# Kernel optimization log

Hardware: AMD Instinct MI355X
Metric: run time of the kernel (lower is better)

## Reference

```python
import jax, jax.numpy as jnp
import numpy as np

EPS = 1e-5  # BatchNorm1d default eps


def _gcn(h_in, W, b, src, dst, dinv):
    h = h_in @ W  # [N, D]
    coef = dinv[src] * dinv[dst]  # [E]
    agg = jax.ops.segment_sum(h[src] * coef[:, None], dst, num_segments=h.shape[0])
    agg = agg + h * (dinv * dinv)[:, None]  # self-loop contribution
    return agg + b


def _bn(h, gamma, beta):
    # training-mode BatchNorm1d over the node dimension (biased variance)
    mu = jnp.mean(h, axis=0)
    var = jnp.var(h, axis=0)
    return gamma * (h - mu) * jax.lax.rsqrt(var + EPS) + beta


def setup_inputs() -> dict:
    key = jax.random.key(0)
    N, E, F_IN, D, B = 50000, 800000, 64, 256, 1000
    ks = jax.random.split(key, 8)
    x = jax.random.normal(ks[0], (N, F_IN), dtype=jnp.float32)
    edge_index = jax.random.randint(ks[1], (2, E), 0, N)
    batch_index = (jnp.arange(N) * B) // N  # sorted, every graph non-empty (~50 nodes each)
    s = lambda k, sh: (jax.random.normal(k, sh, dtype=jnp.float32) * 0.05)
    inp = {
        "x": x, "edge_index": edge_index, "batch_index": batch_index, "num_graphs": B,
        "W0": s(ks[2], (F_IN, D)), "b0": jnp.zeros((D,), jnp.float32),
        "W1": s(ks[3], (D, D)), "b1": jnp.zeros((D,), jnp.float32),
        "W2": s(ks[4], (D, D)), "b2": jnp.zeros((D,), jnp.float32),
        "W3": s(ks[5], (D, D)), "b3": jnp.zeros((D,), jnp.float32),
        "g0": jnp.ones((D,), jnp.float32), "be0": jnp.zeros((D,), jnp.float32),
        "g1": jnp.ones((D,), jnp.float32), "be1": jnp.zeros((D,), jnp.float32),
        "g2": jnp.ones((D,), jnp.float32), "be2": jnp.zeros((D,), jnp.float32),
        "g3": jnp.ones((D,), jnp.float32), "be3": jnp.zeros((D,), jnp.float32),
        "Wout": s(ks[6], (2 * D, 1)), "bout": jnp.zeros((1,), jnp.float32),
    }
    return inp


def reference(x, edge_index, batch_index, num_graphs,
              W0, b0, W1, b1, W2, b2, W3, b3,
              g0, be0, g1, be1, g2, be2, g3, be3,
              Wout, bout):
    N = x.shape[0]
    src, dst = edge_index[0], edge_index[1]
    # degree after adding self-loops (all edge weights = 1)
    deg = 1.0 + jax.ops.segment_sum(jnp.ones(src.shape[0], x.dtype), dst, num_segments=N)
    dinv = jax.lax.rsqrt(deg)

    h = x
    for W, b, g, be in ((W0, b0, g0, be0), (W1, b1, g1, be1),
                        (W2, b2, g2, be2), (W3, b3, g3, be3)):
        h = jnp.tanh(_bn(_gcn(h, W, b, src, dst, dinv), g, be))

    # global max pool + global average pool over graphs
    hmax = jax.ops.segment_max(h, batch_index, num_segments=num_graphs)
    hsum = jax.ops.segment_sum(h, batch_index, num_segments=num_graphs)
    cnt = jax.ops.segment_sum(jnp.ones(N, x.dtype), batch_index, num_segments=num_graphs)
    hmean = hsum / cnt[:, None]
    hidden = jnp.concatenate([hmax, hmean], axis=1)  # [B, 512]
    out = hidden @ Wout + bout  # [B, 1]
    return (out, hidden)
```

## Files before the change

kernel.cpp:

```cpp
#include <hip/hip_runtime.h>
#include <hip/hip_bf16.h>
#include <math.h>

#define D 256
#define EPS 1e-5f
#define SCAN_NB 256

typedef _Float16 f16;
typedef _Float16 f16x4 __attribute__((ext_vector_type(4)));
typedef _Float16 f16x8 __attribute__((ext_vector_type(8)));
typedef float f32x4v __attribute__((ext_vector_type(4)));
typedef unsigned int uint;

__device__ __forceinline__ float fast_tanh(float x) {
    float e = __expf(2.f * x);
    return 1.f - __fdividef(2.f, e + 1.f);
}

union HU { f16 h; unsigned short u; };
__device__ __forceinline__ uint pack_rec(int s, float c) {
    HU hu; hu.h = (f16)c;
    return ((uint)s << 16) | (uint)hu.u;
}
__device__ __forceinline__ float rec_coef(uint r) {
    HU hu; hu.u = (unsigned short)(r & 0xffffu);
    return (float)hu.h;
}

__global__ void k_count(const int* __restrict__ dst, int* __restrict__ cnt,
                        int* __restrict__ rank, int E) {
    int e = blockIdx.x * blockDim.x + threadIdx.x;
    if (e < E) rank[e] = atomicAdd(&cnt[dst[e]], 1);
}

__global__ void k_scan_part(const int* __restrict__ cnt, int* __restrict__ row_ptr,
                            int* __restrict__ partial, int N, int C) {
    __shared__ int sdata[256];
    int b = blockIdx.x, t = threadIdx.x;
    int base = b * C;
    int end = base + C; if (end > N) end = N;
    int running = 0;
    for (int ts = base; ts < end; ts += 256) {
        int idx = ts + t;
        int val = (idx < end) ? cnt[idx] : 0;
        sdata[t] = val;
        __syncthreads();
        for (int s = 1; s < 256; s <<= 1) {
            int v = (t >= s) ? sdata[t - s] : 0;
            __syncthreads();
            sdata[t] += v;
            __syncthreads();
        }
        if (idx < end) row_ptr[idx] = running + sdata[t] - val;
        running += sdata[255];
        __syncthreads();
    }
    if (t == 0) partial[b] = running;
}

__global__ void k_scan_off(int* __restrict__ partial) {
    __shared__ int sdata[256];
    int t = threadIdx.x;
    int val = partial[t];
    sdata[t] = val;
    __syncthreads();
    for (int s = 1; s < 256; s <<= 1) {
        int v = (t >= s) ? sdata[t - s] : 0;
        __syncthreads();
        sdata[t] += v;
        __syncthreads();
    }
    partial[t] = sdata[t] - val;
}

__global__ void k_scan_add(int* __restrict__ row_ptr,
                           const int* __restrict__ partial, const int* __restrict__ cnt,
                           float* __restrict__ dinv, int N, int C, int E) {
    int i = blockIdx.x * 256 + threadIdx.x;
    if (i < N) {
        row_ptr[i] += partial[i / C];
        dinv[i] = rsqrtf(1.0f + (float)cnt[i]);
    }
    if (i == N) row_ptr[N] = E;
}

__global__ void k_fill(const int* __restrict__ src, const int* __restrict__ dst,
                       const int* __restrict__ rank, const int* __restrict__ row_ptr,
                       const float* __restrict__ dinv, uint* __restrict__ ecp, int E) {
    int e = blockIdx.x * blockDim.x + threadIdx.x;
    if (e >= E) return;
    int s = src[e], t = dst[e];
    ecp[row_ptr[t] + rank[e]] = pack_rec(s, dinv[s] * dinv[t]);
}

__global__ void k_cast(const float* __restrict__ in, f16* __restrict__ o, int n4,
                       float* __restrict__ sums, float* __restrict__ sumsq) {
    int i = blockIdx.x * 256 + threadIdx.x;
    if (blockIdx.x == 0) {
        sums[threadIdx.x]  = 0.f;
        sumsq[threadIdx.x] = 0.f;
    }
    if (i >= n4) return;
    float4 v = ((const float4*)in)[i];
    f16x4 h = {(f16)v.x, (f16)v.y, (f16)v.z, (f16)v.w};
    ((f16x4*)o)[i] = h;
}

__global__ void k_prep_w_all(const float* __restrict__ W0, const float* __restrict__ W1,
                             const float* __restrict__ W2, const float* __restrict__ W3,
                             f16* __restrict__ T0, f16* __restrict__ T1,
                             f16* __restrict__ T2, f16* __restrict__ T3) {
    int idx = blockIdx.x * 256 + threadIdx.x;
    if (idx < 16384) {
        int k = idx >> 8, d = idx & 255;
        T0[(size_t)d * 64 + k] = (f16)W0[idx];
        return;
    }
    idx -= 16384;
    const float* W; f16* T;
    if (idx < 65536)      { W = W1; T = T1; }
    else if (idx < 131072){ W = W2; T = T2; idx -= 65536; }
    else                  { W = W3; T = T3; idx -= 131072; }
    int k = idx >> 8, d = idx & 255;
    T[(size_t)d * 256 + k] = (f16)W[idx];
}

#define KSTEP 64
#define ATS 72
__global__ __launch_bounds__(256)
void k_gemm(const f16* __restrict__ A, const f16* __restrict__ Wt,
            f16* __restrict__ outh, int N, int K,
            float* __restrict__ sums, float* __restrict__ sumsq) {
    __shared__ __align__(16) f16 As[128 * ATS];
    __shared__ __align__(16) f16 Bs[128 * ATS];
    const int r0 = blockIdx.x * 128;
    const int c0 = blockIdx.y * 128;
    const int t = threadIdx.x;
    const int lane = t & 63, wave = t >> 6;
    const int wr = wave >> 1, wc = wave & 1;
    const int quad = lane >> 4, m = lane & 15;

    f32x4v acc[4][4];
#pragma unroll
    for (int i = 0; i < 4; ++i)
#pragma unroll
        for (int j = 0; j < 4; ++j) acc[i][j] = {0.f, 0.f, 0.f, 0.f};

    const int sr = t >> 1;
    const int sc0 = (t & 1) * 32;

    for (int k0 = 0; k0 < K; k0 += KSTEP) {
        int gr = r0 + sr;
        uint4 a[4];
#pragma unroll
        for (int u = 0; u < 4; ++u) a[u] = make_uint4(0u, 0u, 0u, 0u);
        if (gr < N) {
            const f16* ap = A + (size_t)gr * K + k0 + sc0;
#pragma unroll
            for (int u = 0; u < 4; ++u) a[u] = *(const uint4*)(ap + u * 8);
        }
#pragma unroll
        for (int u = 0; u < 4; ++u)
            *(uint4*)(As + sr * ATS + sc0 + u * 8) = a[u];
        const f16* bp = Wt + (size_t)(c0 + sr) * K + k0 + sc0;
#pragma unroll
        for (int u = 0; u < 4; ++u)
            *(uint4*)(Bs + sr * ATS + sc0 + u * 8) = *(const uint4*)(bp + u * 8);
        __syncthreads();

#pragma unroll
        for (int kk = 0; kk < KSTEP; kk += 32) {
            f16x8 af[4], bf[4];
#pragma unroll
            for (int i = 0; i < 4; ++i)
                af[i] = *(const f16x8*)(As + (wr * 64 + i * 16 + m) * ATS + kk + quad * 8);
#pragma unroll
            for (int j = 0; j < 4; ++j)
                bf[j] = *(const f16x8*)(Bs + (wc * 64 + j * 16 + m) * ATS + kk + quad * 8);
#pragma unroll
            for (int i = 0; i < 4; ++i)
#pragma unroll
                for (int j = 0; j < 4; ++j)
                    acc[i][j] = __builtin_amdgcn_mfma_f32_16x16x32_f16(af[i], bf[j], acc[i][j], 0, 0, 0);
        }
        __syncthreads();
    }

#pragma unroll
    for (int i = 0; i < 4; ++i) {
#pragma unroll
        for (int r = 0; r < 4; ++r) {
            int row = r0 + wr * 64 + i * 16 + quad * 4 + r;
            if (row < N) {
#pragma unroll
                for (int j = 0; j < 4; ++j) {
                    int colm = c0 + wc * 64 + j * 16 + m;
                    outh[(size_t)row * D + colm] = (f16)acc[i][j][r];
                }
            }
        }
    }

    {
        __shared__ float cs[128], css[128];
        if (t < 128) { cs[t] = 0.f; css[t] = 0.f; }
        __syncthreads();
#pragma unroll
        for (int j = 0; j < 4; ++j) {
            int f = wc * 64 + j * 16 + m;
            float s = 0.f, q = 0.f;
#pragma unroll
            for (int i = 0; i < 4; ++i)
#pragma unroll
                for (int r = 0; r < 4; ++r) {
                    float v = acc[i][j][r];
                    s += v; q += v * v;
                }
            atomicAdd(&cs[f], s);
            atomicAdd(&css[f], q);
        }
        __syncthreads();
        if (t < 128) {
            atomicAdd(&sums[c0 + t], cs[t]);
            atomicAdd(&sumsq[c0 + t], css[t]);
        }
    }
}

__global__ __launch_bounds__(256)
void k_gather_q(const int* __restrict__ row_ptr, const uint4* __restrict__ ecp4,
                const unsigned char* __restrict__ hq, const float* __restrict__ dinv,
                f16* __restrict__ out, float* __restrict__ sums,
                float* __restrict__ sumsq, float* __restrict__ scf_out,
                const float* __restrict__ scf_in, int N) {
    sums[threadIdx.x]  = 0.f;
    sumsq[threadIdx.x] = 0.f;

    const int lane = threadIdx.x & 63;
    const int wave = threadIdx.x >> 6;
    const uint* __restrict__ hqu = (const uint*)hq;
    f16x4* __restrict__ out4 = (f16x4*)out;

    const int wtotal = gridDim.x * 4;
    int i = blockIdx.x * 4 + wave;
    if (i >= N) return;

    int lo = row_ptr[i], hi = row_ptr[i + 1];
    float dv = dinv[i];
    float sci = scf_in ? scf_in[i] : 0.f;
    uint selfu = hqu[(uint)i * 64u + (uint)lane];

    while (true) {
        int inext = i + wtotal;
        int lo2 = 0, hi2 = 0; float dv2 = 0.f, sci2 = 0.f; uint su2 = 0u;
        if (inext < N) {
            lo2 = row_ptr[inext]; hi2 = row_ptr[inext + 1];
            dv2 = dinv[inext];
            if (scf_in) sci2 = scf_in[inext];
            su2 = hqu[(uint)inext * 64u + (uint)lane];
        }

        float dd = dv * dv;
        float scf = scf_in ? sci : dd;
        float4 acc;
        acc.x = (float)(selfu & 0xffu) * dd;
        acc.y = (float)((selfu >> 8) & 0xffu) * dd;
        acc.z = (float)((selfu >> 16) & 0xffu) * dd;
        acc.w = (float)(selfu >> 24) * dd;

        for (int e = (lo & ~3); e < hi; e += 8) {
            uint4 p0 = ecp4[(e >> 2)];
            uint4 p1 = ecp4[(e >> 2) + 1];
            uint pr[8] = {p0.x, p0.y, p0.z, p0.w, p1.x, p1.y, p1.z, p1.w};
            uint rv[8]; float cf[8];
            if ((e >= lo) & (e + 8 <= hi)) {
#pragma unroll
                for (int j = 0; j < 8; ++j) {
                    uint rec = __builtin_amdgcn_readfirstlane(pr[j]);
                    const uint* rp = hqu + ((rec >> 16) << 6);
                    rv[j] = rp[lane];
                    cf[j] = rec_coef(rec);
                }
            } else {
#pragma unroll
                for (int j = 0; j < 8; ++j) {
                    int ej = e + j;
                    bool v = (ej >= lo) & (ej < hi);
                    uint rec = __builtin_amdgcn_readfirstlane(pr[j]);
                    const uint* rp = hqu + ((rec >> 16) << 6);
                    rv[j] = rp[lane];
                    cf[j] = v ? rec_coef(rec) : 0.f;
                }
            }
#pragma unroll
            for (int j = 0; j < 8; ++j) {
                float c = cf[j];
                uint v = rv[j];
                acc.x = fmaf((float)(v & 0xffu), c, acc.x);
                acc.y = fmaf((float)((v >> 8) & 0xffu), c, acc.y);
                acc.z = fmaf((float)((v >> 16) & 0xffu), c, acc.z);
                acc.w = fmaf((float)(v >> 24), c, acc.w);
            }
            if (!scf_in) {
#pragma unroll
                for (int j = 0; j < 8; ++j) scf += cf[j];
            }
        }

        acc.x = fmaf(-128.f, scf, acc.x);
        acc.y = fmaf(-128.f, scf, acc.y);
        acc.z = fmaf(-128.f, scf, acc.z);
        acc.w = fmaf(-128.f, scf, acc.w);

        f16x4 o = {(f16)acc.x, (f16)acc.y, (f16)acc.z, (f16)acc.w};
        out4[(uint)i * 64u + (uint)lane] = o;
        if (scf_out && lane == 0) scf_out[i] = scf;

        if (inext >= N) break;
        i = inext; lo = lo2; hi = hi2; dv = dv2; sci = sci2; selfu = su2;
    }
}

__global__ __launch_bounds__(256)
void k_gather64(const int* __restrict__ row_ptr, const uint4* __restrict__ ecp4,
                const f16* __restrict__ xh, const float* __restrict__ dinv,
                f16* __restrict__ aggx, int N) {
    const int lane = threadIdx.x & 63;
    const int wave = threadIdx.x >> 6;
    const int q = lane >> 4, m = lane & 15;
    const f16x4* __restrict__ x4 = (const f16x4*)xh;
    f16x4* __restrict__ o4 = (f16x4*)aggx;

    int slot   = blockIdx.x * 4 + wave;
    int stride = gridDim.x * 4;
    for (int i0 = slot * 4; i0 < N; i0 += stride * 4) {
        int i = i0 + q;
        bool act = i < N;
        int ii = act ? i : 0;
        int lo = act ? row_ptr[ii] : 0;
        int hi = act ? row_ptr[ii + 1] : 0;
        float dd = act ? dinv[ii] : 0.f; dd *= dd;
        f16x4 hv = act ? x4[(uint)ii * 16u + (uint)m] : (f16x4){0, 0, 0, 0};
        float4 acc;
        acc.x = (float)hv[0] * dd; acc.y = (float)hv[1] * dd;
        acc.z = (float)hv[2] * dd; acc.w = (float)hv[3] * dd;

        for (int e = (lo & ~3); e < hi; e += 8) {
            uint4 p0 = ecp4[(e >> 2)];
            uint4 p1 = ecp4[(e >> 2) + 1];
            uint pr[8] = {p0.x, p0.y, p0.z, p0.w, p1.x, p1.y, p1.z, p1.w};
            int nd[8]; float cf[8];
#pragma unroll
            for (int j = 0; j < 8; ++j) {
                int ej = e + j;
                bool v = (ej >= lo) & (ej < hi);
                nd[j] = v ? (int)(pr[j] >> 16) : ii;
                cf[j] = v ? rec_coef(pr[j]) : 0.f;
            }
            f16x4 r[8];
#pragma unroll
            for (int j = 0; j < 8; ++j) r[j] = x4[(uint)nd[j] * 16u + (uint)m];
#pragma unroll
            for (int j = 0; j < 8; ++j) {
                acc.x = fmaf((float)r[j][0], cf[j], acc.x);
                acc.y = fmaf((float)r[j][1], cf[j], acc.y);
                acc.z = fmaf((float)r[j][2], cf[j], acc.z);
                acc.w = fmaf((float)r[j][3], cf[j], acc.w);
            }
        }
        if (act) {
            f16x4 o = {(f16)acc.x, (f16)acc.y, (f16)acc.z, (f16)acc.w};
            o4[(uint)i * 16u + (uint)m] = o;
        }
    }
}

__global__ __launch_bounds__(256)
void k_bn_tanh_q(const f16* __restrict__ h, const float* __restrict__ sums,
                 const float* __restrict__ sumsq, const float* __restrict__ g,
                 const float* __restrict__ be, float Ninv,
                 unsigned char* __restrict__ hq, int N) {
    const int t = threadIdx.x;
    const int d0 = (t & 31) * 8;
    const int rs = t >> 5;

    float s[8], sh[8];
#pragma unroll
    for (int j = 0; j < 8; ++j) {
        float mu  = sums[d0 + j] * Ninv;
        float var = sumsq[d0 + j] * Ninv - mu * mu;
        float sc  = g[d0 + j] * rsqrtf(var + EPS);
        s[j]  = sc;
        sh[j] = be[d0 + j] - mu * sc;
    }

    const int rstride = gridDim.x * 8;
    for (int r = blockIdx.x * 8 + rs; r < N; r += rstride) {
        f16x8 v = *(const f16x8*)(h + (size_t)r * D + d0);
        uint b[8];
#pragma unroll
        for (int j = 0; j < 8; ++j) {
            float tv = fast_tanh(fmaf((float)v[j], s[j], sh[j]));
            b[j] = (uint)(__float2int_rn(tv * 127.f) + 128);
        }
        uint2 o;
        o.x = b[0] | (b[1] << 8) | (b[2] << 16) | (b[3] << 24);
        o.y = b[4] | (b[5] << 8) | (b[6] << 16) | (b[7] << 24);
        *(uint2*)(hq + (size_t)r * D + d0) = o;
    }
}

__device__ __forceinline__ int lb(const int* __restrict__ a, int n, int v) {
    int lo = 0, hi = n;
    while (lo < hi) {
        int mid = (lo + hi) >> 1;
        if (a[mid] < v) lo = mid + 1; else hi = mid;
    }
    return lo;
}

__global__ void k_pool(const f16* __restrict__ hw, const float* __restrict__ sums,
                       const float* __restrict__ sumsq, const float* __restrict__ gg,
                       const float* __restrict__ be, float Ninv,
                       const int* __restrict__ batch,
                       const float* __restrict__ Wout, const float* __restrict__ bout,
                       float* __restrict__ out, float* __restrict__ hidden, int N) {
    int g = blockIdx.x;
    int d = threadIdx.x;
    float mu  = sums[d] * Ninv;
    float var = sumsq[d] * Ninv - mu * mu;
    float sc  = gg[d] * rsqrtf(var + EPS);
    float sh  = be[d] - mu * sc;

    int lo = lb(batch, N, g);
    int hi = lb(batch, N, g + 1);
    float mx = -INFINITY, sm = 0.0f;
    for (int i = lo; i < hi; ++i) {
        float v = fast_tanh(fmaf((float)hw[(size_t)i * D + d], sc, sh));
        mx = fmaxf(mx, v);
        sm += v;
    }
    float mean = sm / (float)(hi - lo);
    hidden[(size_t)g * (2 * D) + d] = mx;
    hidden[(size_t)g * (2 * D) + D + d] = mean;

    float p = mx * Wout[d] + mean * Wout[D + d];
    __shared__ float red[256];
    red[d] = p;
    __syncthreads();
    for (int s = 128; s > 0; s >>= 1) {
        if (d < s) red[d] += red[d + s];
        __syncthreads();
    }
    if (d == 0) out[g] = red[0] + bout[0];
}

extern "C" void kernel_launch(void* const* d_in, const int* in_sizes, int n_in,
                              void* d_out, int out_size, void* d_ws, size_t ws_size,
                              hipStream_t stream) {
    const float* x          = (const float*)d_in[0];
    const int*   edge_index = (const int*)d_in[1];
    const int*   batch      = (const int*)d_in[2];
    const float* Wl[4] = {(const float*)d_in[4], (const float*)d_in[6],
                          (const float*)d_in[8], (const float*)d_in[10]};
    const float* gl[4]  = {(const float*)d_in[12], (const float*)d_in[14],
                           (const float*)d_in[16], (const float*)d_in[18]};
    const float* bel[4] = {(const float*)d_in[13], (const float*)d_in[15],
                           (const float*)d_in[17], (const float*)d_in[19]};
    const float* Wout = (const float*)d_in[20];
    const float* bout = (const float*)d_in[21];

    const int N = in_sizes[0] / 64;
    const int E = in_sizes[1] / 2;
    const int B = out_size / (1 + 2 * D);

    const int* srcv = edge_index;
    const int* dstv = edge_index + E;

    f16*   hw_h    = (f16*)d_ws;
    f16*   hh      = hw_h + (size_t)N * D;
    f16*   agg_h   = hh + (size_t)N * D;
    f16*   xh      = agg_h + (size_t)N * D;
    f16*   aggx    = xh + (size_t)N * 64;
    f16*   Wt0     = aggx + (size_t)N * 64;
    f16*   Wt1     = Wt0 + 256 * 64;
    f16*   Wt2     = Wt1 + 256 * 256;
    f16*   Wt3     = Wt2 + 256 * 256;
    float* dinv    = (float*)(Wt3 + 256 * 256);
    float* sums    = dinv + N;
    float* sumsq   = sums + D;
    float* scfs    = sumsq + D;
    uint*  ecp     = (uint*)(scfs + N);
    int*   rank    = (int*)(ecp + E + 16);
    int*   cnt     = rank + E;
    int*   row_ptr = cnt + N;
    int*   partial = row_ptr + N + 1;

    unsigned char* hq = (unsigned char*)hh;
    const uint4* ecp4 = (const uint4*)ecp;

    float* out_p    = (float*)d_out;
    float* hidden_p = out_p + B;

    hipMemsetAsync(cnt, 0, (size_t)N * sizeof(int), stream);
    k_count<<<(E + 255) / 256, 256, 0, stream>>>(dstv, cnt, rank, E);
    const int C = (N + SCAN_NB - 1) / SCAN_NB;
    k_scan_part<<<SCAN_NB, 256, 0, stream>>>(cnt, row_ptr, partial, N, C);
    k_scan_off<<<1, 256, 0, stream>>>(partial);
    k_scan_add<<<(N + 1 + 255) / 256, 256, 0, stream>>>(row_ptr, partial,
                                                        cnt, dinv, N, C, E);
    k_fill<<<(E + 255) / 256, 256, 0, stream>>>(srcv, dstv, rank, row_ptr,
                                                dinv, ecp, E);

    k_cast<<<(N * 64 / 4 + 255) / 256, 256, 0, stream>>>(x, xh, N * 64 / 4, sums, sumsq);
    k_prep_w_all<<<(16384 + 3 * 65536 + 255) / 256, 256, 0, stream>>>(
        Wl[0], Wl[1], Wl[2], Wl[3], Wt0, Wt1, Wt2, Wt3);

    const dim3 gemm_grid((N + 127) / 128, 2);
    const float Ninv = 1.0f / (float)N;
    const int bn_grid = (N + 7) / 8;
    f16* Wts[4] = {Wt0, Wt1, Wt2, Wt3};

    k_gather64<<<2048, 256, 0, stream>>>(row_ptr, ecp4, xh, dinv, aggx, N);
    k_gemm<<<gemm_grid, 256, 0, stream>>>(aggx, Wt0, hw_h, N, 64, sums, sumsq);
    k_bn_tanh_q<<<bn_grid, 256, 0, stream>>>(
        hw_h, sums, sumsq, gl[0], bel[0], Ninv, hq, N);

    for (int l = 1; l < 4; ++l) {
        k_gather_q<<<4096, 256, 0, stream>>>(row_ptr, ecp4, hq, dinv,
                                             agg_h, sums, sumsq,
                                             (l == 1) ? scfs : nullptr,
                                             (l > 1) ? scfs : nullptr, N);
        k_gemm<<<gemm_grid, 256, 0, stream>>>(agg_h, Wts[l], hw_h, N, 256,
                                              sums, sumsq);
        if (l < 3) {
            k_bn_tanh_q<<<bn_grid, 256, 0, stream>>>(
                hw_h, sums, sumsq, gl[l], bel[l], Ninv, hq, N);
        }
    }

    k_pool<<<B, 256, 0, stream>>>(hw_h, sums, sumsq, gl[3], bel[3], Ninv,
                                  batch, Wout, bout, out_p, hidden_p, N);
}
```

Measured before the change: 515.4 us.

## Load GEMM tiles directly into LDS with XOR swizzle and padded rows

The GEMM now stages A and W tiles with global_load_lds, a direct global-to-LDS copy that skips the round trip through registers. The padded LDS layout is replaced by an XOR-swizzled layout to avoid bank conflicts. Row bounds checks are dropped by padding the activation buffers to a multiple of 128 rows and zeroing the padding rows. This adds two memsets and relies on the padded workspace, and the BN statistics in the epilogue now also see the padded rows.

```diff
diff --git a/kernel.cpp b/kernel.cpp
--- a/kernel.cpp
+++ b/kernel.cpp
@@ -25,6 +25,12 @@
 __device__ __forceinline__ float rec_coef(uint r) {
     HU hu; hu.u = (unsigned short)(r & 0xffffu);
     return (float)hu.h;
+}
+
+__device__ __forceinline__ void cp16(f16* lds, const f16* g) {
+    __builtin_amdgcn_global_load_lds(
+        (const __attribute__((address_space(1))) unsigned int*)g,
+        (__attribute__((address_space(3))) unsigned int*)lds, 16, 0, 0);
 }
 
 __global__ void k_count(const int* __restrict__ dst, int* __restrict__ cnt,
@@ -126,13 +132,12 @@
 }
 
 #define KSTEP 64
-#define ATS 72
 __global__ __launch_bounds__(256)
 void k_gemm(const f16* __restrict__ A, const f16* __restrict__ Wt,
-            f16* __restrict__ outh, int N, int K,
+            f16* __restrict__ outh, int K,
             float* __restrict__ sums, float* __restrict__ sumsq) {
-    __shared__ __align__(16) f16 As[128 * ATS];
-    __shared__ __align__(16) f16 Bs[128 * ATS];
+    __shared__ __align__(16) f16 As[128 * 64];
+    __shared__ __align__(16) f16 Bs[128 * 64];
     const int r0 = blockIdx.x * 128;
     const int c0 = blockIdx.y * 128;
     const int t = threadIdx.x;
@@ -146,37 +151,41 @@
 #pragma unroll
         for (int j = 0; j < 4; ++j) acc[i][j] = {0.f, 0.f, 0.f, 0.f};
 
-    const int sr = t >> 1;
-    const int sc0 = (t & 1) * 32;
+    int aoff[4], boff[4], loff[4];
+#pragma unroll
+    for (int u = 0; u < 4; ++u) {
+        int idx = u * 256 + t;
+        int row = idx >> 3;
+        int s   = (idx & 7) ^ (row & 7);
+        aoff[u] = (r0 + row) * K + s * 8;
+        boff[u] = (c0 + row) * K + s * 8;
+        loff[u] = (u * 256 + (t & ~63)) * 8;
+    }
 
     for (int k0 = 0; k0 < K; k0 += KSTEP) {
-        int gr = r0 + sr;
-        uint4 a[4];
-#pragma unroll
-        for (int u = 0; u < 4; ++u) a[u] = make_uint4(0u, 0u, 0u, 0u);
-        if (gr < N) {
-            const f16* ap = A + (size_t)gr * K + k0 + sc0;
-#pragma unroll
-            for (int u = 0; u < 4; ++u) a[u] = *(const uint4*)(ap + u * 8);
-        }
 #pragma unroll
         for (int u = 0; u < 4; ++u)
-            *(uint4*)(As + sr * ATS + sc0 + u * 8) = a[u];
-        const f16* bp = Wt + (size_t)(c0 + sr) * K + k0 + sc0;
+            cp16(As + loff[u], A + (size_t)aoff[u] + k0);
 #pragma unroll
         for (int u = 0; u < 4; ++u)
-            *(uint4*)(Bs + sr * ATS + sc0 + u * 8) = *(const uint4*)(bp + u * 8);
-        __syncthreads();
-
-#pragma unroll
-        for (int kk = 0; kk < KSTEP; kk += 32) {
+            cp16(Bs + loff[u], Wt + (size_t)boff[u] + k0);
+        __syncthreads();
+
+#pragma unroll
+        for (int kk = 0; kk < 2; ++kk) {
             f16x8 af[4], bf[4];
 #pragma unroll
-            for (int i = 0; i < 4; ++i)
-                af[i] = *(const f16x8*)(As + (wr * 64 + i * 16 + m) * ATS + kk + quad * 8);
-#pragma unroll
-            for (int j = 0; j < 4; ++j)
-                bf[j] = *(const f16x8*)(Bs + (wc * 64 + j * 16 + m) * ATS + kk + quad * 8);
+            for (int i = 0; i < 4; ++i) {
+                int row = wr * 64 + i * 16 + m;
+                int s   = (kk * 4 + quad) ^ (row & 7);
+                af[i] = *(const f16x8*)((const char*)As + row * 128 + (s << 4));
+            }
+#pragma unroll
+            for (int j = 0; j < 4; ++j) {
+                int row = wc * 64 + j * 16 + m;
+                int s   = (kk * 4 + quad) ^ (row & 7);
+                bf[j] = *(const f16x8*)((const char*)Bs + row * 128 + (s << 4));
+            }
 #pragma unroll
             for (int i = 0; i < 4; ++i)
 #pragma unroll
@@ -191,12 +200,10 @@
 #pragma unroll
         for (int r = 0; r < 4; ++r) {
             int row = r0 + wr * 64 + i * 16 + quad * 4 + r;
-            if (row < N) {
-#pragma unroll
-                for (int j = 0; j < 4; ++j) {
-                    int colm = c0 + wc * 64 + j * 16 + m;
-                    outh[(size_t)row * D + colm] = (f16)acc[i][j][r];
-                }
+#pragma unroll
+            for (int j = 0; j < 4; ++j) {
+                int colm = c0 + wc * 64 + j * 16 + m;
+                outh[(size_t)row * D + colm] = (f16)acc[i][j][r];
             }
         }
     }
@@ -473,16 +480,18 @@
     const int N = in_sizes[0] / 64;
     const int E = in_sizes[1] / 2;
     const int B = out_size / (1 + 2 * D);
+    const int NB   = (N + 127) / 128;
+    const int NPAD = NB * 128;
 
     const int* srcv = edge_index;
     const int* dstv = edge_index + E;
 
     f16*   hw_h    = (f16*)d_ws;
-    f16*   hh      = hw_h + (size_t)N * D;
+    f16*   hh      = hw_h + (size_t)NPAD * D;
     f16*   agg_h   = hh + (size_t)N * D;
-    f16*   xh      = agg_h + (size_t)N * D;
+    f16*   xh      = agg_h + (size_t)NPAD * D;
     f16*   aggx    = xh + (size_t)N * 64;
-    f16*   Wt0     = aggx + (size_t)N * 64;
+    f16*   Wt0     = aggx + (size_t)NPAD * 64;
     f16*   Wt1     = Wt0 + 256 * 64;
     f16*   Wt2     = Wt1 + 256 * 256;
     f16*   Wt3     = Wt2 + 256 * 256;
@@ -503,6 +512,8 @@
     float* hidden_p = out_p + B;
 
     hipMemsetAsync(cnt, 0, (size_t)N * sizeof(int), stream);
+    hipMemsetAsync(agg_h + (size_t)N * D, 0, (size_t)(NPAD - N) * D * sizeof(f16), stream);
+    hipMemsetAsync(aggx + (size_t)N * 64, 0, (size_t)(NPAD - N) * 64 * sizeof(f16), stream);
     k_count<<<(E + 255) / 256, 256, 0, stream>>>(dstv, cnt, rank, E);
     const int C = (N + SCAN_NB - 1) / SCAN_NB;
     k_scan_part<<<SCAN_NB, 256, 0, stream>>>(cnt, row_ptr, partial, N, C);
@@ -516,13 +527,13 @@
     k_prep_w_all<<<(16384 + 3 * 65536 + 255) / 256, 256, 0, stream>>>(
         Wl[0], Wl[1], Wl[2], Wl[3], Wt0, Wt1, Wt2, Wt3);
 
-    const dim3 gemm_grid((N + 127) / 128, 2);
+    const dim3 gemm_grid(NB, 2);
     const float Ninv = 1.0f / (float)N;
     const int bn_grid = (N + 7) / 8;
     f16* Wts[4] = {Wt0, Wt1, Wt2, Wt3};
 
     k_gather64<<<2048, 256, 0, stream>>>(row_ptr, ecp4, xh, dinv, aggx, N);
-    k_gemm<<<gemm_grid, 256, 0, stream>>>(aggx, Wt0, hw_h, N, 64, sums, sumsq);
+    k_gemm<<<gemm_grid, 256, 0, stream>>>(aggx, Wt0, hw_h, 64, sums, sumsq);
     k_bn_tanh_q<<<bn_grid, 256, 0, stream>>>(
         hw_h, sums, sumsq, gl[0], bel[0], Ninv, hq, N);
 
@@ -531,7 +542,7 @@
                                              agg_h, sums, sumsq,
                                              (l == 1) ? scfs : nullptr,
                                              (l > 1) ? scfs : nullptr, N);
-        k_gemm<<<gemm_grid, 256, 0, stream>>>(agg_h, Wts[l], hw_h, N, 256,
+        k_gemm<<<gemm_grid, 256, 0, stream>>>(agg_h, Wts[l], hw_h, 256,
                                               sums, sumsq);
         if (l < 3) {
             k_bn_tanh_q<<<bn_grid, 256, 0, stream>>>(
```

Result: no change. 507.0 us (-1.6%).
